# Optimization experiments

Measured on AMD Instinct MI355X. Metric: run time of the kernel, lower is better.

The kernel has to match this reference:

```python
import jax, jax.numpy as jnp
import numpy as np

N = 100_000      # total nodes
E = 1_600_000    # total edges
G = 32           # number of graphs in batch
IN = 100         # in_channels
H = 64           # hidden_channels
L = 3            # num_layers
EPS = 1e-5       # BatchNorm eps


def setup_inputs() -> dict:
    key = jax.random.key(0)
    ks = jax.random.split(key, 16)
    x = jax.random.normal(ks[0], (N, IN), jnp.float32)
    edge_index = jax.random.randint(ks[1], (2, E), 0, N)
    edge_weight = jax.random.uniform(ks[2], (E,), jnp.float32)
    batch = jnp.sort(jax.random.randint(ks[3], (N,), 0, G))
    inp = {"x": x, "edge_index": edge_index, "edge_weight": edge_weight, "batch": batch}
    dims = [IN] + [H] * L
    for i in range(L):
        din, dout = dims[i], dims[i + 1]
        s = 1.0 / np.sqrt(din)
        inp[f"W{i}"] = jax.random.uniform(ks[4 + i], (din, dout), jnp.float32, -s, s)
        inp[f"b{i}"] = jnp.zeros((dout,), jnp.float32)
        inp[f"g{i}"] = jnp.ones((dout,), jnp.float32)   # BN gamma
        inp[f"bt{i}"] = jnp.zeros((dout,), jnp.float32)  # BN beta
        inp[f"rm{i}"] = jnp.zeros((dout,), jnp.float32)  # BN running mean
        inp[f"rv{i}"] = jnp.ones((dout,), jnp.float32)   # BN running var
    return inp


def reference(x, edge_index, edge_weight, batch,
              W0, b0, g0, bt0, rm0, rv0,
              W1, b1, g1, bt1, rm1, rv1,
              W2, b2, g2, bt2, rm2, rv2):
    n = x.shape[0]
    loop = jnp.arange(n)
    src = jnp.concatenate([edge_index[0], loop])
    dst = jnp.concatenate([edge_index[1], loop])
    w = jnp.concatenate([jnp.abs(edge_weight), jnp.ones((n,), x.dtype)])
    # symmetric GCN normalization (deg computed on target / col)
    deg = jax.ops.segment_sum(w, dst, num_segments=n)
    deg_safe = jnp.where(deg > 0, deg, 1.0)
    dinv = jnp.where(deg > 0, jax.lax.rsqrt(deg_safe), 0.0)
    norm = dinv[src] * w * dinv[dst]  # [E+N]

    def gcn_bn_relu(h, W, b, g, bt, rm, rv):
        h = h @ W                              # [N, dout]
        msg = h[src] * norm[:, None]           # gather + scale
        h = jax.ops.segment_sum(msg, dst, num_segments=n) + b  # scatter-add
        h = (h - rm) * jax.lax.rsqrt(rv + EPS) * g + bt        # BN (eval)
        return jnp.maximum(h, 0.0)             # ReLU (dropout off in eval)

    h = x
    for (W, b, g, bt, rm, rv) in [(W0, b0, g0, bt0, rm0, rv0),
                                  (W1, b1, g1, bt1, rm1, rv1),
                                  (W2, b2, g2, bt2, rm2, rv2)]:
        h = gcn_bn_relu(h, W, b, g, bt, rm, rv)

    # mean+add global pooling
    s = jax.ops.segment_sum(h, batch, num_segments=G)
    cnt = jax.ops.segment_sum(jnp.ones((n,), h.dtype), batch, num_segments=G)
    mean = s / jnp.maximum(cnt, 1.0)[:, None]
    return jnp.concatenate([mean, s], axis=-1)  # [G, 2*H]
```

## Files before the change

kernel.cpp:

```cpp
#include <hip/hip_runtime.h>
#include <hip/hip_bf16.h>

#define NN 100000
#define EE 1600000
#define GG 32
#define INC 100
#define HC 64
#define CAP 64
#define BN_EPS 1e-5f
#define NB_POOL 1563
#define WQ 32767.0f
#define NSLICE 8
#define SLICE_N 12500
#define EBLK 6250

typedef __hip_bfloat16 bf16;

__device__ __forceinline__ float bflo(unsigned u) { return __uint_as_float(u << 16); }
__device__ __forceinline__ float bfhi(unsigned u) { return __uint_as_float(u & 0xffff0000u); }
__device__ __forceinline__ unsigned f2bf(float f) {
    unsigned x = __float_as_uint(f);
    return (x + 0x7fffu + ((x >> 16) & 1u)) >> 16;
}
__device__ __forceinline__ unsigned bfpack(float lo, float hi) {
    return f2bf(lo) | (f2bf(hi) << 16);
}


__global__ __launch_bounds__(256) void k_scatter_ell(const int* __restrict__ ei,
                                                     const float* __restrict__ ew,
                                                     int* __restrict__ cur,
                                                     unsigned* __restrict__ epk) {
    unsigned b = blockIdx.x;
    int slice = b & (NSLICE - 1);
    int e = (int)(b >> 3) * 256 + threadIdx.x;
    if (e >= EE) return;
    int d = __builtin_nontemporal_load(&ei[EE + e]);
    int lo = slice * SLICE_N;
    if (d < lo || d >= lo + SLICE_N) return;
    int s = __builtin_nontemporal_load(&ei[e]);
    float w = __builtin_nontemporal_load(&ew[e]);
    int qw = (int)(fabsf(w) * WQ + 0.5f);
    if (qw > 32767) qw = 32767;
    int slot = atomicAdd(&cur[d], 1);
    if (slot < CAP)
        epk[(size_t)d * CAP + slot] = ((unsigned)s << 15) | (unsigned)qw;
}


__global__ __launch_bounds__(256) void k_dinv_ell(const int* __restrict__ cur,
                                                  const unsigned* __restrict__ epk,
                                                  float* __restrict__ dinv,
                                                  float* __restrict__ pool_s,
                                                  float* __restrict__ pool_c) {
    if (blockIdx.x == 0) {
        for (int i = threadIdx.x; i < GG * 64 + GG; i += 256) {
            if (i < GG * 64) pool_s[i] = 0.f;
            else             pool_c[i - GG * 64] = 0.f;
        }
    }
    int wid = (blockIdx.x * 256 + threadIdx.x) >> 6;
    int lane = threadIdx.x & 63;
    if (wid >= NN) return;
    int cnt = min(cur[wid], CAP);
    float v = 0.f;
    if (lane < cnt)
        v = (float)(epk[(size_t)wid * CAP + lane] & 0x7fffu) * (1.0f / WQ);
    for (int o = 32; o > 0; o >>= 1) v += __shfl_down(v, o);
    if (lane == 0) dinv[wid] = rsqrtf(v + 1.0f);
}


__device__ __forceinline__ float ldf(const float* p, size_t i) { return p[i]; }
__device__ __forceinline__ float ldf(const bf16* p, size_t i) { return __bfloat162float(p[i]); }

template <int DIN, typename Tin>
__global__ __launch_bounds__(256) void k_gemm(const Tin* __restrict__ X,
                                              const float* __restrict__ W,
                                              const float* __restrict__ dinv,
                                              bf16* __restrict__ Y) {
    __shared__ float Ws[DIN * 64];
    __shared__ float Xs[32 * DIN];
    int row0 = blockIdx.x * 32;
    for (int idx = threadIdx.x; idx < DIN * 64; idx += 256)
        Ws[idx] = W[idx];
    for (int idx = threadIdx.x; idx < 32 * DIN; idx += 256) {
        int r = idx / DIN, k = idx - r * DIN;
        Xs[idx] = ldf(X, (size_t)(row0 + r) * DIN + k);
    }
    __syncthreads();
    int c = threadIdx.x & 63;
    int r0 = threadIdx.x >> 6;
    float acc[8];
#pragma unroll
    for (int j = 0; j < 8; j++) acc[j] = 0.f;
    for (int k = 0; k < DIN; k++) {
        float wv = Ws[k * 64 + c];
#pragma unroll
        for (int j = 0; j < 8; j++)
            acc[j] += Xs[(r0 + j * 4) * DIN + k] * wv;
    }
#pragma unroll
    for (int j = 0; j < 8; j++) {
        int row = row0 + r0 + j * 4;
        Y[(size_t)row * 64 + c] = __float2bfloat16(acc[j] * dinv[row]);
    }
}


__global__ __launch_bounds__(256) void k_gather_gemm(
    const unsigned* __restrict__ hw32, const int* __restrict__ cur,
    const unsigned* __restrict__ epk, const float* __restrict__ dinv,
    const float* __restrict__ bb, const float* __restrict__ gg,
    const float* __restrict__ btp, const float* __restrict__ rmp,
    const float* __restrict__ rvp, const float* __restrict__ W,
    unsigned* __restrict__ out32) {
    __shared__ float Ws[64 * 64];
    __shared__ float hs[8][64];
    int tid = threadIdx.x;
    for (int idx = tid; idx < 64 * 64; idx += 256)
        Ws[idx] = W[idx];

    int lane = tid & 63;
    int l5 = lane & 31;
    int local = (tid >> 6) * 2 + (lane >> 5);
    int n = blockIdx.x * 8 + local;
    float di = dinv[n];
    unsigned us = hw32[(size_t)n * 32 + l5];
    float a0 = bflo(us), b0 = bfhi(us);
    float a1 = 0.f, b1 = 0.f, a2 = 0.f, b2 = 0.f;
    float a3 = 0.f, b3 = 0.f, a4 = 0.f, b4 = 0.f;
    int cnt = min(cur[n], CAP);
    const unsigned* ce = epk + (size_t)n * CAP;
    const float q = 1.0f / WQ;
    unsigned klo = (l5 < cnt) ? ce[l5] : 0u;
    unsigned khi = 0u;
    if (cnt > 32) khi = (32 + l5 < cnt) ? ce[32 + l5] : 0u;
    int p = 0;
    for (; p + 8 <= cnt; p += 8) {
        unsigned base = (p < 32) ? klo : khi;
        int pb = p & 31;
        unsigned k0 = __shfl(base, pb + 0, 32);
        unsigned k1 = __shfl(base, pb + 1, 32);
        unsigned k2 = __shfl(base, pb + 2, 32);
        unsigned k3 = __shfl(base, pb + 3, 32);
        unsigned k4 = __shfl(base, pb + 4, 32);
        unsigned k5 = __shfl(base, pb + 5, 32);
        unsigned k6 = __shfl(base, pb + 6, 32);
        unsigned k7 = __shfl(base, pb + 7, 32);
        unsigned u0 = hw32[(size_t)(k0 >> 15) * 32 + l5];
        unsigned u1 = hw32[(size_t)(k1 >> 15) * 32 + l5];
        unsigned u2 = hw32[(size_t)(k2 >> 15) * 32 + l5];
        unsigned u3 = hw32[(size_t)(k3 >> 15) * 32 + l5];
        unsigned u4 = hw32[(size_t)(k4 >> 15) * 32 + l5];
        unsigned u5 = hw32[(size_t)(k5 >> 15) * 32 + l5];
        unsigned u6 = hw32[(size_t)(k6 >> 15) * 32 + l5];
        unsigned u7 = hw32[(size_t)(k7 >> 15) * 32 + l5];
        float c0 = (float)(k0 & 0x7fffu) * q, c1 = (float)(k1 & 0x7fffu) * q;
        float c2 = (float)(k2 & 0x7fffu) * q, c3 = (float)(k3 & 0x7fffu) * q;
        float c4 = (float)(k4 & 0x7fffu) * q, c5 = (float)(k5 & 0x7fffu) * q;
        float c6 = (float)(k6 & 0x7fffu) * q, c7 = (float)(k7 & 0x7fffu) * q;
        a0 += bflo(u0) * c0; b0 += bfhi(u0) * c0;
        a1 += bflo(u1) * c1; b1 += bfhi(u1) * c1;
        a2 += bflo(u2) * c2; b2 += bfhi(u2) * c2;
        a3 += bflo(u3) * c3; b3 += bfhi(u3) * c3;
        a4 += bflo(u4) * c4; b4 += bfhi(u4) * c4;
        a0 += bflo(u5) * c5; b0 += bfhi(u5) * c5;
        a1 += bflo(u6) * c6; b1 += bfhi(u6) * c6;
        a2 += bflo(u7) * c7; b2 += bfhi(u7) * c7;
    }
    for (; p + 4 <= cnt; p += 4) {
        unsigned base = (p < 32) ? klo : khi;
        int pb = p & 31;
        unsigned k0 = __shfl(base, pb + 0, 32);
        unsigned k1 = __shfl(base, pb + 1, 32);
        unsigned k2 = __shfl(base, pb + 2, 32);
        unsigned k3 = __shfl(base, pb + 3, 32);
        unsigned u0 = hw32[(size_t)(k0 >> 15) * 32 + l5];
        unsigned u1 = hw32[(size_t)(k1 >> 15) * 32 + l5];
        unsigned u2 = hw32[(size_t)(k2 >> 15) * 32 + l5];
        unsigned u3 = hw32[(size_t)(k3 >> 15) * 32 + l5];
        float c0 = (float)(k0 & 0x7fffu) * q, c1 = (float)(k1 & 0x7fffu) * q;
        float c2 = (float)(k2 & 0x7fffu) * q, c3 = (float)(k3 & 0x7fffu) * q;
        a0 += bflo(u0) * c0; b0 += bfhi(u0) * c0;
        a1 += bflo(u1) * c1; b1 += bfhi(u1) * c1;
        a2 += bflo(u2) * c2; b2 += bfhi(u2) * c2;
        a3 += bflo(u3) * c3; b3 += bfhi(u3) * c3;
    }
    for (; p < cnt; ++p) {
        unsigned base = (p < 32) ? klo : khi;
        unsigned k0 = __shfl(base, p & 31, 32);
        unsigned u0 = hw32[(size_t)(k0 >> 15) * 32 + l5];
        float c0 = (float)(k0 & 0x7fffu) * q;
        a0 += bflo(u0) * c0; b0 += bfhi(u0) * c0;
    }
    int cl = l5 * 2, ch = cl + 1;
    float alo = (((a0 + a1) + (a2 + a3)) + a4) * di + bb[cl];
    float ahi = (((b0 + b1) + (b2 + b3)) + b4) * di + bb[ch];
    float slo = gg[cl] * rsqrtf(rvp[cl] + BN_EPS);
    float shi = gg[ch] * rsqrtf(rvp[ch] + BN_EPS);
    hs[local][cl] = fmaxf((alo - rmp[cl]) * slo + btp[cl], 0.f);
    hs[local][ch] = fmaxf((ahi - rmp[ch]) * shi + btp[ch], 0.f);
    __syncthreads();

    int r = tid >> 5;
    int pr = tid & 31;
    int c2 = pr * 2;
    float accl = 0.f, acch = 0.f;
#pragma unroll 8
    for (int k = 0; k < 64; ++k) {
        float h = hs[r][k];
        accl += h * Ws[k * 64 + c2];
        acch += h * Ws[k * 64 + c2 + 1];
    }
    int rn = blockIdx.x * 8 + r;
    float dib = dinv[rn];
    out32[(size_t)rn * 32 + pr] = bfpack(accl * dib, acch * dib);
}


__global__ __launch_bounds__(256) void k_gather_bn(
    const unsigned* __restrict__ hw32, const int* __restrict__ cur,
    const unsigned* __restrict__ epk, const float* __restrict__ dinv,
    const float* __restrict__ bb, const float* __restrict__ gg,
    const float* __restrict__ btp, const float* __restrict__ rmp,
    const float* __restrict__ rvp, unsigned* __restrict__ ho32) {
    int wave = (blockIdx.x * 256 + threadIdx.x) >> 6;
    int lane = threadIdx.x & 63;
    int n = wave * 2 + (lane >> 5);
    int l5 = lane & 31;
    if (n >= NN) return;
    float di = dinv[n];
    unsigned us = hw32[(size_t)n * 32 + l5];
    float a0 = bflo(us), b0 = bfhi(us);
    float a1 = 0.f, b1 = 0.f, a2 = 0.f, b2 = 0.f;
    float a3 = 0.f, b3 = 0.f, a4 = 0.f, b4 = 0.f;
    int cnt = min(cur[n], CAP);
    const unsigned* ce = epk + (size_t)n * CAP;
    const float q = 1.0f / WQ;
    unsigned klo = (l5 < cnt) ? ce[l5] : 0u;
    unsigned khi = 0u;
    if (cnt > 32) khi = (32 + l5 < cnt) ? ce[32 + l5] : 0u;
    int p = 0;
    for (; p + 8 <= cnt; p += 8) {
        unsigned base = (p < 32) ? klo : khi;
        int pb = p & 31;
        unsigned k0 = __shfl(base, pb + 0, 32);
        unsigned k1 = __shfl(base, pb + 1, 32);
        unsigned k2 = __shfl(base, pb + 2, 32);
        unsigned k3 = __shfl(base, pb + 3, 32);
        unsigned k4 = __shfl(base, pb + 4, 32);
        unsigned k5 = __shfl(base, pb + 5, 32);
        unsigned k6 = __shfl(base, pb + 6, 32);
        unsigned k7 = __shfl(base, pb + 7, 32);
        unsigned u0 = hw32[(size_t)(k0 >> 15) * 32 + l5];
        unsigned u1 = hw32[(size_t)(k1 >> 15) * 32 + l5];
        unsigned u2 = hw32[(size_t)(k2 >> 15) * 32 + l5];
        unsigned u3 = hw32[(size_t)(k3 >> 15) * 32 + l5];
        unsigned u4 = hw32[(size_t)(k4 >> 15) * 32 + l5];
        unsigned u5 = hw32[(size_t)(k5 >> 15) * 32 + l5];
        unsigned u6 = hw32[(size_t)(k6 >> 15) * 32 + l5];
        unsigned u7 = hw32[(size_t)(k7 >> 15) * 32 + l5];
        float c0 = (float)(k0 & 0x7fffu) * q, c1 = (float)(k1 & 0x7fffu) * q;
        float c2 = (float)(k2 & 0x7fffu) * q, c3 = (float)(k3 & 0x7fffu) * q;
        float c4 = (float)(k4 & 0x7fffu) * q, c5 = (float)(k5 & 0x7fffu) * q;
        float c6 = (float)(k6 & 0x7fffu) * q, c7 = (float)(k7 & 0x7fffu) * q;
        a0 += bflo(u0) * c0; b0 += bfhi(u0) * c0;
        a1 += bflo(u1) * c1; b1 += bfhi(u1) * c1;
        a2 += bflo(u2) * c2; b2 += bfhi(u2) * c2;
        a3 += bflo(u3) * c3; b3 += bfhi(u3) * c3;
        a4 += bflo(u4) * c4; b4 += bfhi(u4) * c4;
        a0 += bflo(u5) * c5; b0 += bfhi(u5) * c5;
        a1 += bflo(u6) * c6; b1 += bfhi(u6) * c6;
        a2 += bflo(u7) * c7; b2 += bfhi(u7) * c7;
    }
    for (; p + 4 <= cnt; p += 4) {
        unsigned base = (p < 32) ? klo : khi;
        int pb = p & 31;
        unsigned k0 = __shfl(base, pb + 0, 32);
        unsigned k1 = __shfl(base, pb + 1, 32);
        unsigned k2 = __shfl(base, pb + 2, 32);
        unsigned k3 = __shfl(base, pb + 3, 32);
        unsigned u0 = hw32[(size_t)(k0 >> 15) * 32 + l5];
        unsigned u1 = hw32[(size_t)(k1 >> 15) * 32 + l5];
        unsigned u2 = hw32[(size_t)(k2 >> 15) * 32 + l5];
        unsigned u3 = hw32[(size_t)(k3 >> 15) * 32 + l5];
        float c0 = (float)(k0 & 0x7fffu) * q, c1 = (float)(k1 & 0x7fffu) * q;
        float c2 = (float)(k2 & 0x7fffu) * q, c3 = (float)(k3 & 0x7fffu) * q;
        a0 += bflo(u0) * c0; b0 += bfhi(u0) * c0;
        a1 += bflo(u1) * c1; b1 += bfhi(u1) * c1;
        a2 += bflo(u2) * c2; b2 += bfhi(u2) * c2;
        a3 += bflo(u3) * c3; b3 += bfhi(u3) * c3;
    }
    for (; p < cnt; ++p) {
        unsigned base = (p < 32) ? klo : khi;
        unsigned k0 = __shfl(base, p & 31, 32);
        unsigned u0 = hw32[(size_t)(k0 >> 15) * 32 + l5];
        float c0 = (float)(k0 & 0x7fffu) * q;
        a0 += bflo(u0) * c0; b0 += bfhi(u0) * c0;
    }
    int cl = l5 * 2, ch = cl + 1;
    float alo = (((a0 + a1) + (a2 + a3)) + a4) * di + bb[cl];
    float ahi = (((b0 + b1) + (b2 + b3)) + b4) * di + bb[ch];
    float slo = gg[cl] * rsqrtf(rvp[cl] + BN_EPS);
    float shi = gg[ch] * rsqrtf(rvp[ch] + BN_EPS);
    float olo = fmaxf((alo - rmp[cl]) * slo + btp[cl], 0.f);
    float ohi = fmaxf((ahi - rmp[ch]) * shi + btp[ch], 0.f);
    ho32[(size_t)n * 32 + l5] = bfpack(olo, ohi);
}


__global__ __launch_bounds__(64) void k_pool(const bf16* __restrict__ h,
                                             const int* __restrict__ batch,
                                             float* __restrict__ s, float* __restrict__ cntf) {
    int c = threadIdx.x;
    int n0 = blockIdx.x * 64;
    if (n0 >= NN) return;
    int n1 = n0 + 64; if (n1 > NN) n1 = NN;
    float acc = 0.f, cnt = 0.f;
    int gcur = batch[n0];
    for (int i = n0; i < n1; ++i) {
        int gi = batch[i];
        if (gi != gcur) {
            atomicAdd(&s[gcur * 64 + c], acc);
            if (c == 0) atomicAdd(&cntf[gcur], cnt);
            acc = 0.f; cnt = 0.f; gcur = gi;
        }
        acc += __bfloat162float(h[(size_t)i * 64 + c]);
        cnt += 1.f;
    }
    atomicAdd(&s[gcur * 64 + c], acc);
    if (c == 0) atomicAdd(&cntf[gcur], cnt);
}


__global__ void k_out(const float* __restrict__ s, const float* __restrict__ cntf,
                      float* __restrict__ out) {
    int idx = blockIdx.x * 256 + threadIdx.x;
    if (idx >= GG * 128) return;
    int g = idx >> 7, c = idx & 127;
    float v;
    if (c < 64) v = s[g * 64 + c] / fmaxf(cntf[g], 1.f);
    else        v = s[g * 64 + (c - 64)];
    out[idx] = v;
}


extern "C" void kernel_launch(void* const* d_in, const int* in_sizes, int n_in,
                              void* d_out, int out_size, void* d_ws, size_t ws_size,
                              hipStream_t stream) {
    const float* x   = (const float*)d_in[0];
    const int* ei    = (const int*)d_in[1];
    const float* ew  = (const float*)d_in[2];
    const int* batch = (const int*)d_in[3];
    const float *Wp[3], *bp[3], *gp[3], *btp[3], *rmp[3], *rvp[3];
    for (int l = 0; l < 3; ++l) {
        Wp[l]  = (const float*)d_in[4 + 6 * l + 0];
        bp[l]  = (const float*)d_in[4 + 6 * l + 1];
        gp[l]  = (const float*)d_in[4 + 6 * l + 2];
        btp[l] = (const float*)d_in[4 + 6 * l + 3];
        rmp[l] = (const float*)d_in[4 + 6 * l + 4];
        rvp[l] = (const float*)d_in[4 + 6 * l + 5];
    }

    size_t off = 0;
    auto carve = [&](size_t bytes) {
        void* r = (char*)d_ws + off;
        off += (bytes + 255) & ~(size_t)255;
        return r;
    };
    int*      cur    = (int*)     carve(NN * 4);
    float*    dinv   = (float*)   carve(NN * 4);
    unsigned* epk    = (unsigned*)carve((size_t)NN * CAP * 4);
    bf16*     hw     = (bf16*)    carve((size_t)NN * 64 * 2);
    bf16*     ha     = (bf16*)    carve((size_t)NN * 64 * 2);
    float*    pool_s = (float*)   carve(GG * 64 * 4);
    float*    pool_c = (float*)   carve(GG * 4);

    hipMemsetAsync(cur, 0, NN * 4, stream);

    int nwblk  = (NN * 64 + 255) / 256;
    int gatblk = NN / 8;
    int gemm_grid = NN / 32;

    k_scatter_ell<<<EBLK * NSLICE, 256, 0, stream>>>(ei, ew, cur, epk);
    k_dinv_ell<<<nwblk, 256, 0, stream>>>(cur, epk, dinv, pool_s, pool_c);

    k_gemm<INC, float><<<gemm_grid, 256, 0, stream>>>(x, Wp[0], dinv, hw);
    k_gather_gemm<<<gatblk, 256, 0, stream>>>((unsigned*)hw, cur, epk, dinv,
                                              bp[0], gp[0], btp[0], rmp[0], rvp[0],
                                              Wp[1], (unsigned*)ha);
    k_gather_gemm<<<gatblk, 256, 0, stream>>>((unsigned*)ha, cur, epk, dinv,
                                              bp[1], gp[1], btp[1], rmp[1], rvp[1],
                                              Wp[2], (unsigned*)hw);
    k_gather_bn<<<gatblk, 256, 0, stream>>>((unsigned*)hw, cur, epk, dinv,
                                            bp[2], gp[2], btp[2], rmp[2], rvp[2], (unsigned*)ha);

    k_pool<<<NB_POOL, 64, 0, stream>>>(ha, batch, pool_s, pool_c);
    k_out<<<(GG * 128 + 255) / 256, 256, 0, stream>>>(pool_s, pool_c, (float*)d_out);
}
```

Before: 463.6 us.

## Fuse layer-0 GEMM into edge scatter kernel and apply dinv scaling later

The layer-0 projection x@W0 moves into the same launch as the ELL edge scatter, using separate block ranges, so the dense compute can overlap the atomic-bound scatter. The degree-normalisation scale and bf16 packing move into the dinv kernel, which now reads an fp32 intermediate. This removes one launch and the dependence of the GEMM on dinv. The cost is an extra fp32 buffer written and read back, and the GEMM now reads x straight from global memory without LDS staging.

```diff
diff --git a/kernel.cpp b/kernel.cpp
--- a/kernel.cpp
+++ b/kernel.cpp
@@ -12,7 +12,8 @@
 #define WQ 32767.0f
 #define NSLICE 8
 #define SLICE_N 12500
-#define EBLK 6250
+#define NGEMM 3125
+#define NSCAT 50000
 
 typedef __hip_bfloat16 bf16;
 
@@ -27,13 +28,38 @@
 }
 
 
-__global__ __launch_bounds__(256) void k_scatter_ell(const int* __restrict__ ei,
-                                                     const float* __restrict__ ew,
-                                                     int* __restrict__ cur,
-                                                     unsigned* __restrict__ epk) {
+__global__ __launch_bounds__(256) void k_scatter_gemm0(
+    const int* __restrict__ ei, const float* __restrict__ ew,
+    int* __restrict__ cur, unsigned* __restrict__ epk,
+    const float* __restrict__ x, const float* __restrict__ W0,
+    float* __restrict__ h0raw) {
+    __shared__ float Ws[INC * 64];
     unsigned b = blockIdx.x;
+    if (b < NGEMM) {
+        int row0 = (int)b * 32;
+        for (int idx = threadIdx.x; idx < INC * 64; idx += 256)
+            Ws[idx] = W0[idx];
+        __syncthreads();
+        int c = threadIdx.x & 63;
+        int r0 = threadIdx.x >> 6;
+        float acc[8];
+#pragma unroll
+        for (int j = 0; j < 8; j++) acc[j] = 0.f;
+        const float* xb = x + (size_t)row0 * INC;
+        for (int k = 0; k < INC; k++) {
+            float wv = Ws[k * 64 + c];
+#pragma unroll
+            for (int j = 0; j < 8; j++)
+                acc[j] += xb[(size_t)(r0 + j * 4) * INC + k] * wv;
+        }
+#pragma unroll
+        for (int j = 0; j < 8; j++)
+            h0raw[(size_t)(row0 + r0 + j * 4) * 64 + c] = acc[j];
+        return;
+    }
+    unsigned bb = b - NGEMM;
     int slice = b & (NSLICE - 1);
-    int e = (int)(b >> 3) * 256 + threadIdx.x;
+    int e = (int)(bb >> 3) * 256 + threadIdx.x;
     if (e >= EE) return;
     int d = __builtin_nontemporal_load(&ei[EE + e]);
     int lo = slice * SLICE_N;
@@ -48,11 +74,11 @@
 }
 
 
-__global__ __launch_bounds__(256) void k_dinv_ell(const int* __restrict__ cur,
-                                                  const unsigned* __restrict__ epk,
-                                                  float* __restrict__ dinv,
-                                                  float* __restrict__ pool_s,
-                                                  float* __restrict__ pool_c) {
+__global__ __launch_bounds__(256) void k_dinv_scale(
+    const int* __restrict__ cur, const unsigned* __restrict__ epk,
+    float* __restrict__ dinv, const float* __restrict__ h0raw,
+    unsigned* __restrict__ hw32out,
+    float* __restrict__ pool_s, float* __restrict__ pool_c) {
     if (blockIdx.x == 0) {
         for (int i = threadIdx.x; i < GG * 64 + GG; i += 256) {
             if (i < GG * 64) pool_s[i] = 0.f;
@@ -67,43 +93,12 @@
     if (lane < cnt)
         v = (float)(epk[(size_t)wid * CAP + lane] & 0x7fffu) * (1.0f / WQ);
     for (int o = 32; o > 0; o >>= 1) v += __shfl_down(v, o);
-    if (lane == 0) dinv[wid] = rsqrtf(v + 1.0f);
-}
-
-
-__device__ __forceinline__ float ldf(const float* p, size_t i) { return p[i]; }
-__device__ __forceinline__ float ldf(const bf16* p, size_t i) { return __bfloat162float(p[i]); }
-
-template <int DIN, typename Tin>
-__global__ __launch_bounds__(256) void k_gemm(const Tin* __restrict__ X,
-                                              const float* __restrict__ W,
-                                              const float* __restrict__ dinv,
-                                              bf16* __restrict__ Y) {
-    __shared__ float Ws[DIN * 64];
-    __shared__ float Xs[32 * DIN];
-    int row0 = blockIdx.x * 32;
-    for (int idx = threadIdx.x; idx < DIN * 64; idx += 256)
-        Ws[idx] = W[idx];
-    for (int idx = threadIdx.x; idx < 32 * DIN; idx += 256) {
-        int r = idx / DIN, k = idx - r * DIN;
-        Xs[idx] = ldf(X, (size_t)(row0 + r) * DIN + k);
-    }
-    __syncthreads();
-    int c = threadIdx.x & 63;
-    int r0 = threadIdx.x >> 6;
-    float acc[8];
-#pragma unroll
-    for (int j = 0; j < 8; j++) acc[j] = 0.f;
-    for (int k = 0; k < DIN; k++) {
-        float wv = Ws[k * 64 + c];
-#pragma unroll
-        for (int j = 0; j < 8; j++)
-            acc[j] += Xs[(r0 + j * 4) * DIN + k] * wv;
-    }
-#pragma unroll
-    for (int j = 0; j < 8; j++) {
-        int row = row0 + r0 + j * 4;
-        Y[(size_t)row * 64 + c] = __float2bfloat16(acc[j] * dinv[row]);
+    v = __shfl(v, 0);
+    float di = rsqrtf(v + 1.0f);
+    if (lane == 0) dinv[wid] = di;
+    if (lane < 32) {
+        float2 f2 = reinterpret_cast<const float2*>(h0raw)[(size_t)wid * 32 + lane];
+        hw32out[(size_t)wid * 32 + lane] = bfpack(f2.x * di, f2.y * di);
     }
 }
 
@@ -372,6 +367,7 @@
     int*      cur    = (int*)     carve(NN * 4);
     float*    dinv   = (float*)   carve(NN * 4);
     unsigned* epk    = (unsigned*)carve((size_t)NN * CAP * 4);
+    float*    h0raw  = (float*)   carve((size_t)NN * 64 * 4);
     bf16*     hw     = (bf16*)    carve((size_t)NN * 64 * 2);
     bf16*     ha     = (bf16*)    carve((size_t)NN * 64 * 2);
     float*    pool_s = (float*)   carve(GG * 64 * 4);
@@ -381,12 +377,11 @@
 
     int nwblk  = (NN * 64 + 255) / 256;
     int gatblk = NN / 8;
-    int gemm_grid = NN / 32;
-
-    k_scatter_ell<<<EBLK * NSLICE, 256, 0, stream>>>(ei, ew, cur, epk);
-    k_dinv_ell<<<nwblk, 256, 0, stream>>>(cur, epk, dinv, pool_s, pool_c);
-
-    k_gemm<INC, float><<<gemm_grid, 256, 0, stream>>>(x, Wp[0], dinv, hw);
+
+    k_scatter_gemm0<<<NGEMM + NSCAT, 256, 0, stream>>>(ei, ew, cur, epk, x, Wp[0], h0raw);
+    k_dinv_scale<<<nwblk, 256, 0, stream>>>(cur, epk, dinv, h0raw, (unsigned*)hw,
+                                            pool_s, pool_c);
+
     k_gather_gemm<<<gatblk, 256, 0, stream>>>((unsigned*)hw, cur, epk, dinv,
                                               bp[0], gp[0], btp[0], rmp[0], rvp[0],
                                               Wp[1], (unsigned*)ha);
```

Result: slower. 507.8 us (+9.5%).
